# Kernel optimization log

Measured on AMD Instinct MI355X. Metric: run time of the kernel, lower is better.

## Reference

```python
import jax, jax.numpy as jnp
import numpy as np

B, N, DIM = 4, 2048, 512
HEADS, DK = 8, 64
SCALE = DK ** -0.5


def setup_inputs() -> dict:
    key = jax.random.key(0)
    k1, k2, k3, k4 = jax.random.split(key, 4)
    x = jax.random.normal(k1, (B, N, DIM), dtype=jnp.float32)
    # nn.Linear(dim, dim_key*heads, bias=False): y = x @ W.T; store W already transposed
    Wq = jax.random.normal(k2, (DIM, HEADS * DK), dtype=jnp.float32) * (DIM ** -0.5)
    Wk = jax.random.normal(k3, (DIM, HEADS * DK), dtype=jnp.float32) * (DIM ** -0.5)
    rel_content_bias = jax.random.normal(k4, (1, HEADS, 1, DK), dtype=jnp.float32)
    return {"x": x, "Wq": Wq, "Wk": Wk, "rel_content_bias": rel_content_bias}


def _split_heads(t, h):
    # [b, n, h*d] -> [b, h, n, d]
    b, n, hd = t.shape
    return t.reshape(b, n, h, hd // h).transpose(0, 2, 1, 3)


def reference(x, Wq, Wk, rel_content_bias):
    q = _split_heads(x @ Wq, HEADS) * SCALE          # [b, h, n, dk]
    k = _split_heads(x @ Wk, HEADS)                  # [b, h, n, dk]
    v = _split_heads(x, HEADS)                       # [b, h, n, dim/h]
    logits = jnp.einsum('bhid,bhjd->bhij', q + rel_content_bias, k)
    attn = jax.nn.sigmoid(logits)                    # no softmax normalization
    out = jnp.einsum('bhij,bhjd->bhid', attn, v)     # [b, h, n, dim/h]
    b, h, n, d = out.shape
    return out.transpose(0, 2, 1, 3).reshape(b, n, h * d)
```

## Files before the change

### kernel.cpp

```cpp
#include <hip/hip_runtime.h>
#include <hip/hip_bf16.h>
#include <stdint.h>

#define BB 4
#define NN 2048
#define DIMD 512
#define HH 8
#define DKK 64
#define MTOT (BB * NN)
constexpr float SCALE = 0.125f;

typedef __attribute__((ext_vector_type(4))) float f32x4;
typedef __attribute__((ext_vector_type(8))) short bf16x8;
typedef __attribute__((ext_vector_type(4))) _Float16 f16x4;
typedef __attribute__((ext_vector_type(2))) __fp16 fp16v2;
typedef __attribute__((ext_vector_type(4))) __fp16 fp16v4;

__device__ __forceinline__ unsigned short f2bf(float f) {
  union { float f; uint32_t u; } v; v.f = f;
  uint32_t u = v.u;
  return (unsigned short)((u + 0x7FFFu + ((u >> 16) & 1u)) >> 16);
}

__device__ __forceinline__ float sigmoidf(float x) {
  return __builtin_amdgcn_rcpf(1.0f + __expf(-x));
}

__global__ __launch_bounds__(256) void prep_x(const float* __restrict__ x,
                                              unsigned short* __restrict__ xb,
                                              unsigned short* __restrict__ xtf) {
  __shared__ __align__(16) unsigned short T[64][72];
  const int b = blockIdx.z, nt = blockIdx.x, dt = blockIdx.y;
  const int tid = threadIdx.x;
  const int n0 = nt * 64, d0 = dt * 64;
  const float* src = x + ((size_t)b * NN + n0) * DIMD + d0;
#pragma unroll
  for (int r = 0; r < 16; r++) {
    int idx = tid + r * 256;
    int nl = idx >> 6, dl = idx & 63;
    float f = src[(size_t)nl * DIMD + dl];
    xb[((size_t)b * NN + n0 + nl) * DIMD + d0 + dl] = f2bf(f);
    union { _Float16 h; unsigned short u; } c; c.h = (_Float16)f;
    T[dl][nl] = c.u;
  }
  __syncthreads();
  unsigned short* dst = xtf + ((size_t)b * DIMD + d0) * NN + n0;
#pragma unroll
  for (int r = 0; r < 16; r++) {
    int idx = tid + r * 256;
    int dl = idx >> 6, nl = idx & 63;
    dst[(size_t)dl * NN + nl] = T[dl][nl];
  }
}

__global__ __launch_bounds__(256) void prep_w(const float* __restrict__ wq,
                                              const float* __restrict__ wk,
                                              unsigned short* __restrict__ wtq,
                                              unsigned short* __restrict__ wtk) {
  __shared__ __align__(16) unsigned short T[64][72];
  const float* w = blockIdx.z ? wk : wq;
  unsigned short* wt = blockIdx.z ? wtk : wtq;
  const int kt = blockIdx.x, nt = blockIdx.y;
  const int tid = threadIdx.x;
  const int k0 = kt * 64, n0 = nt * 64;
#pragma unroll
  for (int r = 0; r < 16; r++) {
    int idx = tid + r * 256;
    int kl = idx >> 6, nl = idx & 63;
    T[nl][kl] = f2bf(w[(size_t)(k0 + kl) * DIMD + n0 + nl]);
  }
  __syncthreads();
#pragma unroll
  for (int r = 0; r < 16; r++) {
    int idx = tid + r * 256;
    int nl = idx >> 6, kl = idx & 63;
    wt[(size_t)(n0 + nl) * DIMD + k0 + kl] = T[nl][kl];
  }
}

__global__ __launch_bounds__(256) void qk_gemm(const unsigned short* __restrict__ xb,
                                               const unsigned short* __restrict__ wtq,
                                               const unsigned short* __restrict__ wtk,
                                               const float* __restrict__ bias,
                                               unsigned short* __restrict__ qout,
                                               unsigned short* __restrict__ kout) {
  __shared__ __align__(16) unsigned short Als[128][72];
  __shared__ __align__(16) unsigned short Bls[128][72];
  const int mb = blockIdx.x, nb = blockIdx.y;
  const bool isQ = (nb < 4);
  const unsigned short* wt = isQ ? wtq : wtk;
  unsigned short* outp = isQ ? qout : kout;
  const int n0 = (nb & 3) * 128, m0 = mb * 128;
  const int tid = threadIdx.x;
  const int wave = tid >> 6, lane = tid & 63;
  const int quad = lane >> 4, l16 = lane & 15;
  const int wm = wave >> 1, wn = wave & 1;

  f32x4 acc[4][4];
#pragma unroll
  for (int a = 0; a < 4; a++)
#pragma unroll
    for (int c = 0; c < 4; c++) acc[a][c] = (f32x4){0.f, 0.f, 0.f, 0.f};

  for (int k0 = 0; k0 < DIMD; k0 += 64) {
    __syncthreads();
#pragma unroll
    for (int r = 0; r < 4; r++) {
      int idx = tid + r * 256;
      int row = idx >> 3, c = idx & 7;
      *(uint4*)&Als[row][c * 8] =
          *(const uint4*)(xb + (size_t)(m0 + row) * DIMD + k0 + c * 8);
      *(uint4*)&Bls[row][c * 8] =
          *(const uint4*)(wt + (size_t)(n0 + row) * DIMD + k0 + c * 8);
    }
    __syncthreads();
#pragma unroll
    for (int ks = 0; ks < 2; ks++) {
      bf16x8 af[4], bfr[4];
#pragma unroll
      for (int t = 0; t < 4; t++) {
        af[t] = *(const bf16x8*)&Als[wm * 64 + t * 16 + l16][quad * 8 + ks * 32];
        bfr[t] = *(const bf16x8*)&Bls[wn * 64 + t * 16 + l16][quad * 8 + ks * 32];
      }
#pragma unroll
      for (int tm = 0; tm < 4; tm++)
#pragma unroll
        for (int tn = 0; tn < 4; tn++)
          acc[tm][tn] =
              __builtin_amdgcn_mfma_f32_16x16x32_bf16(af[tm], bfr[tn], acc[tm][tn], 0, 0, 0);
    }
  }
#pragma unroll
  for (int tm = 0; tm < 4; tm++) {
#pragma unroll
    for (int tn = 0; tn < 4; tn++) {
#pragma unroll
      for (int r = 0; r < 4; r++) {
        int row = m0 + wm * 64 + tm * 16 + quad * 4 + r;
        int gcol = n0 + wn * 64 + tn * 16 + l16;
        float v = acc[tm][tn][r];
        if (isQ) v = v * SCALE + bias[gcol];
        outp[(size_t)row * DIMD + gcol] = f2bf(v);
      }
    }
  }
}

__global__ __launch_bounds__(256) void attn(const unsigned short* __restrict__ qb,
                                            const unsigned short* __restrict__ kb,
                                            const unsigned short* __restrict__ xtf,
                                            float* __restrict__ out) {
  __shared__ __align__(16) unsigned short Kls[64][72];
  __shared__ __align__(16) unsigned short Vtls[64][72];
  const int it = blockIdx.x, bh = blockIdx.y;
  const int b = bh >> 3, h = bh & 7;
  const int i0 = it * 128;
  const int tid = threadIdx.x;
  const int wave = tid >> 6, lane = tid & 63;
  const int quad = lane >> 4, l16 = lane & 15;

  bf16x8 qfrag[2][2];
  int irow[2];
#pragma unroll
  for (int s_ = 0; s_ < 2; s_++) {
    irow[s_] = i0 + (wave * 2 + s_) * 16 + l16;
    const unsigned short* qp =
        qb + ((size_t)b * NN + irow[s_]) * DIMD + h * DKK + quad * 8;
    qfrag[s_][0] = *(const bf16x8*)qp;
    qfrag[s_][1] = *(const bf16x8*)(qp + 32);
  }

  f32x4 o[2][4];
#pragma unroll
  for (int s_ = 0; s_ < 2; s_++)
#pragma unroll
    for (int td = 0; td < 4; td++) o[s_][td] = (f32x4){0.f, 0.f, 0.f, 0.f};

  const unsigned short* kbase = kb + (size_t)b * NN * DIMD + h * DKK;
  const unsigned short* vbase = xtf + ((size_t)b * DIMD + h * DKK) * NN;

  for (int j0 = 0; j0 < NN; j0 += 64) {
    __syncthreads();
#pragma unroll
    for (int r = 0; r < 2; r++) {
      int idx = tid + r * 256;
      int row = idx >> 3, c = idx & 7;
      *(uint4*)&Kls[row][c * 8] =
          *(const uint4*)(kbase + (size_t)(j0 + row) * DIMD + c * 8);
      *(uint4*)&Vtls[row][c * 8] =
          *(const uint4*)(vbase + (size_t)row * NN + j0 + c * 8);
    }
    __syncthreads();

    f16x4 pfrag[2][4];
#pragma unroll
    for (int t = 0; t < 4; t++) {
      bf16x8 kf0 = *(const bf16x8*)&Kls[t * 16 + l16][quad * 8];
      bf16x8 kf1 = *(const bf16x8*)&Kls[t * 16 + l16][quad * 8 + 32];
#pragma unroll
      for (int s_ = 0; s_ < 2; s_++) {
        f32x4 sv = (f32x4){0.f, 0.f, 0.f, 0.f};
        sv = __builtin_amdgcn_mfma_f32_16x16x32_bf16(kf0, qfrag[s_][0], sv, 0, 0, 0);
        sv = __builtin_amdgcn_mfma_f32_16x16x32_bf16(kf1, qfrag[s_][1], sv, 0, 0, 0);
        fp16v2 lo = __builtin_amdgcn_cvt_pkrtz(sigmoidf(sv[0]), sigmoidf(sv[1]));
        fp16v2 hi = __builtin_amdgcn_cvt_pkrtz(sigmoidf(sv[2]), sigmoidf(sv[3]));
        fp16v4 p;
        p.x = lo.x; p.y = lo.y; p.z = hi.x; p.w = hi.y;
        pfrag[s_][t] = __builtin_bit_cast(f16x4, p);
      }
    }

#pragma unroll
    for (int td = 0; td < 4; td++) {
#pragma unroll
      for (int t = 0; t < 4; t++) {
        f16x4 vf = *(const f16x4*)&Vtls[td * 16 + l16][t * 16 + quad * 4];
        o[0][td] = __builtin_amdgcn_mfma_f32_16x16x16f16(vf, pfrag[0][t], o[0][td], 0, 0, 0);
        o[1][td] = __builtin_amdgcn_mfma_f32_16x16x16f16(vf, pfrag[1][t], o[1][td], 0, 0, 0);
      }
    }
  }

#pragma unroll
  for (int s_ = 0; s_ < 2; s_++) {
#pragma unroll
    for (int td = 0; td < 4; td++) {
      float* op = out + ((size_t)b * NN + irow[s_]) * DIMD + h * DKK + td * 16 + quad * 4;
      *(f32x4*)op = o[s_][td];
    }
  }
}

extern "C" void kernel_launch(void* const* d_in, const int* in_sizes, int n_in,
                              void* d_out, int out_size, void* d_ws, size_t ws_size,
                              hipStream_t stream) {
  const float* x = (const float*)d_in[0];
  const float* Wq = (const float*)d_in[1];
  const float* Wk = (const float*)d_in[2];
  const float* bias = (const float*)d_in[3];
  float* out = (float*)d_out;

  unsigned short* ws = (unsigned short*)d_ws;
  unsigned short* xb = ws;
  unsigned short* xtf = xb + (size_t)MTOT * DIMD;
  unsigned short* wtq = xtf + (size_t)MTOT * DIMD;
  unsigned short* wtk = wtq + (size_t)DIMD * DIMD;
  unsigned short* qb = wtk + (size_t)DIMD * DIMD;
  unsigned short* kb = qb + (size_t)MTOT * DIMD;

  prep_x<<<dim3(32, 8, 4), 256, 0, stream>>>(x, xb, xtf);
  prep_w<<<dim3(8, 8, 2), 256, 0, stream>>>(Wq, Wk, wtq, wtk);
  qk_gemm<<<dim3(64, 8), 256, 0, stream>>>(xb, wtq, wtk, bias, qb, kb);
  attn<<<dim3(16, 32), 256, 0, stream>>>(qb, kb, xtf, out);
}
```

Measured before the change: 180.2 us.

## Retile attention to 64 query rows with 128-key tiles; vectorize prep stores

The attention kernel now gives each block 64 query rows, one 16-row strip per wave, and walks keys in 128-wide tiles. The launch grid doubles to 1024 blocks, which raises occupancy and lowers register pressure. Each K/V tile is now reused by half as many queries, so total K/V global traffic doubles while the number of barriers per block halves. The prep kernels switch to 16-byte vectorized stores for the bf16 copy and the transposes; strided shared-memory writes in the transpose may cause bank conflicts.

Result: faster. 174.8 us (-3.0%).

```diff
diff --git a/kernel.cpp b/kernel.cpp
--- a/kernel.cpp
+++ b/kernel.cpp
@@ -16,10 +16,17 @@
 typedef __attribute__((ext_vector_type(2))) __fp16 fp16v2;
 typedef __attribute__((ext_vector_type(4))) __fp16 fp16v4;
 
+union pack8 { unsigned short s[8]; uint4 v; };
+
 __device__ __forceinline__ unsigned short f2bf(float f) {
   union { float f; uint32_t u; } v; v.f = f;
   uint32_t u = v.u;
   return (unsigned short)((u + 0x7FFFu + ((u >> 16) & 1u)) >> 16);
+}
+
+__device__ __forceinline__ unsigned short f2h(float f) {
+  union { _Float16 h; unsigned short u; } c; c.h = (_Float16)f;
+  return c.u;
 }
 
 __device__ __forceinline__ float sigmoidf(float x) {
@@ -35,21 +42,27 @@
   const int n0 = nt * 64, d0 = dt * 64;
   const float* src = x + ((size_t)b * NN + n0) * DIMD + d0;
 #pragma unroll
-  for (int r = 0; r < 16; r++) {
-    int idx = tid + r * 256;
-    int nl = idx >> 6, dl = idx & 63;
-    float f = src[(size_t)nl * DIMD + dl];
-    xb[((size_t)b * NN + n0 + nl) * DIMD + d0 + dl] = f2bf(f);
-    union { _Float16 h; unsigned short u; } c; c.h = (_Float16)f;
-    T[dl][nl] = c.u;
+  for (int r = 0; r < 2; r++) {
+    int idx = tid + r * 256;
+    int nl = idx >> 3, c = idx & 7;
+    const float* sp = src + (size_t)nl * DIMD + c * 8;
+    pack8 pb;
+#pragma unroll
+    for (int k = 0; k < 8; k++) {
+      float f = sp[k];
+      pb.s[k] = f2bf(f);
+      T[c * 8 + k][nl] = f2h(f);
+    }
+    *(uint4*)(xb + ((size_t)b * NN + n0 + nl) * DIMD + d0 + c * 8) = pb.v;
   }
   __syncthreads();
   unsigned short* dst = xtf + ((size_t)b * DIMD + d0) * NN + n0;
 #pragma unroll
-  for (int r = 0; r < 16; r++) {
-    int idx = tid + r * 256;
-    int dl = idx >> 6, nl = idx & 63;
-    dst[(size_t)dl * NN + nl] = T[dl][nl];
+  for (int r = 0; r < 2; r++) {
+    int idx = tid + r * 256;
+    int dl = idx >> 3, c = idx & 7;
+    uint4 v = *(const uint4*)&T[dl][c * 8];
+    *(uint4*)(dst + (size_t)dl * NN + c * 8) = v;
   }
 }
 
@@ -71,10 +84,11 @@
   }
   __syncthreads();
 #pragma unroll
-  for (int r = 0; r < 16; r++) {
-    int idx = tid + r * 256;
-    int nl = idx >> 6, kl = idx & 63;
-    wt[(size_t)(n0 + nl) * DIMD + k0 + kl] = T[nl][kl];
+  for (int r = 0; r < 2; r++) {
+    int idx = tid + r * 256;
+    int nl = idx >> 3, c = idx & 7;
+    uint4 v = *(const uint4*)&T[nl][c * 8];
+    *(uint4*)(wt + (size_t)(n0 + nl) * DIMD + k0 + c * 8) = v;
   }
 }
 
@@ -150,84 +164,68 @@
                                             const unsigned short* __restrict__ kb,
                                             const unsigned short* __restrict__ xtf,
                                             float* __restrict__ out) {
-  __shared__ __align__(16) unsigned short Kls[64][72];
-  __shared__ __align__(16) unsigned short Vtls[64][72];
+  __shared__ __align__(16) unsigned short Kls[128][72];
+  __shared__ __align__(16) unsigned short Vtls[64][136];
   const int it = blockIdx.x, bh = blockIdx.y;
   const int b = bh >> 3, h = bh & 7;
-  const int i0 = it * 128;
+  const int i0 = it * 64;
   const int tid = threadIdx.x;
   const int wave = tid >> 6, lane = tid & 63;
   const int quad = lane >> 4, l16 = lane & 15;
 
-  bf16x8 qfrag[2][2];
-  int irow[2];
-#pragma unroll
-  for (int s_ = 0; s_ < 2; s_++) {
-    irow[s_] = i0 + (wave * 2 + s_) * 16 + l16;
-    const unsigned short* qp =
-        qb + ((size_t)b * NN + irow[s_]) * DIMD + h * DKK + quad * 8;
-    qfrag[s_][0] = *(const bf16x8*)qp;
-    qfrag[s_][1] = *(const bf16x8*)(qp + 32);
-  }
-
-  f32x4 o[2][4];
-#pragma unroll
-  for (int s_ = 0; s_ < 2; s_++)
-#pragma unroll
-    for (int td = 0; td < 4; td++) o[s_][td] = (f32x4){0.f, 0.f, 0.f, 0.f};
+  const int irow = i0 + wave * 16 + l16;
+  bf16x8 qfrag0, qfrag1;
+  {
+    const unsigned short* qp = qb + ((size_t)b * NN + irow) * DIMD + h * DKK + quad * 8;
+    qfrag0 = *(const bf16x8*)qp;
+    qfrag1 = *(const bf16x8*)(qp + 32);
+  }
+
+  f32x4 o[4];
+#pragma unroll
+  for (int td = 0; td < 4; td++) o[td] = (f32x4){0.f, 0.f, 0.f, 0.f};
 
   const unsigned short* kbase = kb + (size_t)b * NN * DIMD + h * DKK;
   const unsigned short* vbase = xtf + ((size_t)b * DIMD + h * DKK) * NN;
 
-  for (int j0 = 0; j0 < NN; j0 += 64) {
-    __syncthreads();
-#pragma unroll
-    for (int r = 0; r < 2; r++) {
+  for (int j0 = 0; j0 < NN; j0 += 128) {
+    __syncthreads();
+#pragma unroll
+    for (int r = 0; r < 4; r++) {
       int idx = tid + r * 256;
       int row = idx >> 3, c = idx & 7;
       *(uint4*)&Kls[row][c * 8] =
           *(const uint4*)(kbase + (size_t)(j0 + row) * DIMD + c * 8);
-      *(uint4*)&Vtls[row][c * 8] =
-          *(const uint4*)(vbase + (size_t)row * NN + j0 + c * 8);
-    }
-    __syncthreads();
-
-    f16x4 pfrag[2][4];
-#pragma unroll
-    for (int t = 0; t < 4; t++) {
+      int rowd = idx >> 4, cv = idx & 15;
+      *(uint4*)&Vtls[rowd][cv * 8] =
+          *(const uint4*)(vbase + (size_t)rowd * NN + j0 + cv * 8);
+    }
+    __syncthreads();
+
+#pragma unroll
+    for (int t = 0; t < 8; t++) {
       bf16x8 kf0 = *(const bf16x8*)&Kls[t * 16 + l16][quad * 8];
       bf16x8 kf1 = *(const bf16x8*)&Kls[t * 16 + l16][quad * 8 + 32];
-#pragma unroll
-      for (int s_ = 0; s_ < 2; s_++) {
-        f32x4 sv = (f32x4){0.f, 0.f, 0.f, 0.f};
-        sv = __builtin_amdgcn_mfma_f32_16x16x32_bf16(kf0, qfrag[s_][0], sv, 0, 0, 0);
-        sv = __builtin_amdgcn_mfma_f32_16x16x32_bf16(kf1, qfrag[s_][1], sv, 0, 0, 0);
-        fp16v2 lo = __builtin_amdgcn_cvt_pkrtz(sigmoidf(sv[0]), sigmoidf(sv[1]));
-        fp16v2 hi = __builtin_amdgcn_cvt_pkrtz(sigmoidf(sv[2]), sigmoidf(sv[3]));
-        fp16v4 p;
-        p.x = lo.x; p.y = lo.y; p.z = hi.x; p.w = hi.y;
-        pfrag[s_][t] = __builtin_bit_cast(f16x4, p);
+      f32x4 sv = (f32x4){0.f, 0.f, 0.f, 0.f};
+      sv = __builtin_amdgcn_mfma_f32_16x16x32_bf16(kf0, qfrag0, sv, 0, 0, 0);
+      sv = __builtin_amdgcn_mfma_f32_16x16x32_bf16(kf1, qfrag1, sv, 0, 0, 0);
+      fp16v2 lo = __builtin_amdgcn_cvt_pkrtz(sigmoidf(sv[0]), sigmoidf(sv[1]));
+      fp16v2 hi = __builtin_amdgcn_cvt_pkrtz(sigmoidf(sv[2]), sigmoidf(sv[3]));
+      fp16v4 p;
+      p.x = lo.x; p.y = lo.y; p.z = hi.x; p.w = hi.y;
+      f16x4 pfrag = __builtin_bit_cast(f16x4, p);
+#pragma unroll
+      for (int td = 0; td < 4; td++) {
+        f16x4 vf = *(const f16x4*)&Vtls[td * 16 + l16][t * 16 + quad * 4];
+        o[td] = __builtin_amdgcn_mfma_f32_16x16x16f16(vf, pfrag, o[td], 0, 0, 0);
       }
     }
-
-#pragma unroll
-    for (int td = 0; td < 4; td++) {
-#pragma unroll
-      for (int t = 0; t < 4; t++) {
-        f16x4 vf = *(const f16x4*)&Vtls[td * 16 + l16][t * 16 + quad * 4];
-        o[0][td] = __builtin_amdgcn_mfma_f32_16x16x16f16(vf, pfrag[0][t], o[0][td], 0, 0, 0);
-        o[1][td] = __builtin_amdgcn_mfma_f32_16x16x16f16(vf, pfrag[1][t], o[1][td], 0, 0, 0);
-      }
-    }
-  }
-
-#pragma unroll
-  for (int s_ = 0; s_ < 2; s_++) {
-#pragma unroll
-    for (int td = 0; td < 4; td++) {
-      float* op = out + ((size_t)b * NN + irow[s_]) * DIMD + h * DKK + td * 16 + quad * 4;
-      *(f32x4*)op = o[s_][td];
-    }
+  }
+
+#pragma unroll
+  for (int td = 0; td < 4; td++) {
+    float* op = out + ((size_t)b * NN + irow) * DIMD + h * DKK + td * 16 + quad * 4;
+    *(f32x4*)op = o[td];
   }
 }
 
@@ -251,5 +249,5 @@
   prep_x<<<dim3(32, 8, 4), 256, 0, stream>>>(x, xb, xtf);
   prep_w<<<dim3(8, 8, 2), 256, 0, stream>>>(Wq, Wk, wtq, wtk);
   qk_gemm<<<dim3(64, 8), 256, 0, stream>>>(xb, wtq, wtk, bias, qb, kb);
-  attn<<<dim3(16, 32), 256, 0, stream>>>(qb, kb, xtf, out);
-}
+  attn<<<dim3(32, 32), 256, 0, stream>>>(qb, kb, xtf, out);
+}
```
